# Optimization experiments

Measured on AMD Instinct MI355X. Metric: run time of the kernel, lower is better.

The kernel has to match this reference:

```python
import jax, jax.numpy as jnp
import numpy as np

# QuantizedLinear (BitNet-style ternary weights).
# The original pack_weights/unpack_weights 2-bit round-trip is an identity on the
# ternary values; the nested-loop ternary_matrix_operation is mathematically
# x @ Q^T (weights stored [out, in], accumulating +x[:,i] / -x[:,i] per +-1 entry).

def setup_inputs() -> dict:
    key = jax.random.key(0)
    k1, k2 = jax.random.split(key)
    TOKENS, IN_F, OUT_F = 8192, 4096, 4096
    x = jax.random.normal(k1, (TOKENS, IN_F), dtype=jnp.float32)
    weight = jax.random.normal(k2, (OUT_F, IN_F), dtype=jnp.float32)
    bias = jnp.zeros((OUT_F,), dtype=jnp.float32)
    return {"x": x, "weight": weight, "bias": bias}

def reference(x, weight, bias):
    # absmean ternary quantization: gamma = mean(|W|) + eps
    gamma = jnp.mean(jnp.abs(weight)) + 1e-5
    q = jnp.clip(jnp.round(weight / gamma), -1.0, 1.0)  # ternary {-1,0,1}, [out,in]
    # pack->unpack 2-bit round-trip is identity; loop accumulation == GEMM
    return jnp.einsum('bi,oi->bo', x, q) + bias
```

## Files before the change

kernel.cpp:

```cpp
#include <hip/hip_runtime.h>
#include <stdint.h>


#define M_DIM 8192
#define N_DIM 4096
#define K_DIM 4096
#define BM 256
#define BN 256
#define BK 64

typedef __attribute__((ext_vector_type(4))) int vi4;

#define BAR() asm volatile("s_barrier" ::: "memory")
#define VMW4() asm volatile("s_waitcnt vmcnt(4)" ::: "memory")
#define VMW0() asm volatile("s_waitcnt vmcnt(0)" ::: "memory")
#define SB0() __builtin_amdgcn_sched_barrier(0)
#define LGKM0()                                             \
  do {                                                      \
    SB0();                                                  \
    asm volatile("s_waitcnt lgkmcnt(0)" ::: "memory");      \
    SB0();                                                  \
  } while (0)

__device__ __forceinline__ void load_lds16(const void* g, void* l) {
  __builtin_amdgcn_global_load_lds(
      (const __attribute__((address_space(1))) void*)g,
      (__attribute__((address_space(3))) void*)l,
      16, 0, 0);
}

__global__ __launch_bounds__(256) void k_abs_partial(const float* __restrict__ w,
                                                     double* __restrict__ partial) {
  const int tid = threadIdx.x;
  const size_t base = (size_t)blockIdx.x * 8192 + (size_t)tid * 4;
  double s = 0.0;
#pragma unroll
  for (int it = 0; it < 8; ++it) {
    const float4 v = *reinterpret_cast<const float4*>(w + base + (size_t)it * 1024);
    s += (double)fabsf(v.x) + (double)fabsf(v.y) + (double)fabsf(v.z) + (double)fabsf(v.w);
  }
  __shared__ double sd[256];
  sd[tid] = s;
  __syncthreads();
  for (int off = 128; off > 0; off >>= 1) {
    if (tid < off) sd[tid] += sd[tid + off];
    __syncthreads();
  }
  if (tid == 0) partial[blockIdx.x] = sd[0];
}

__global__ __launch_bounds__(256) void k_abs_final(const double* __restrict__ partial,
                                                   float* __restrict__ gamma_out) {
  const int tid = threadIdx.x;
  double s = 0.0;
  for (int i = tid; i < 2048; i += 256) s += partial[i];
  __shared__ double sd[256];
  sd[tid] = s;
  __syncthreads();
  for (int off = 128; off > 0; off >>= 1) {
    if (tid < off) sd[tid] += sd[tid + off];
    __syncthreads();
  }
  if (tid == 0) {
    float g = (float)(sd[0] / 16777216.0);
    gamma_out[0] = g + 1e-5f;
  }
}

__global__ __launch_bounds__(256) void k_quant(const float* __restrict__ w,
                                               const float* __restrict__ gamma_p,
                                               int* __restrict__ qb) {
  const float g = gamma_p[0];
  const size_t n4 = (size_t)N_DIM * K_DIM / 4;
  const size_t stride = (size_t)gridDim.x * blockDim.x;
  for (size_t i = (size_t)blockIdx.x * blockDim.x + threadIdx.x; i < n4; i += stride) {
    const float4 v = reinterpret_cast<const float4*>(w)[i];
    float r;
    int a, b, c, d;
    r = rintf(v.x / g); a = (r >= 1.0f) ? 1 : ((r <= -1.0f) ? -1 : 0);
    r = rintf(v.y / g); b = (r >= 1.0f) ? 1 : ((r <= -1.0f) ? -1 : 0);
    r = rintf(v.z / g); c = (r >= 1.0f) ? 1 : ((r <= -1.0f) ? -1 : 0);
    r = rintf(v.w / g); d = (r >= 1.0f) ? 1 : ((r <= -1.0f) ? -1 : 0);
    qb[i] = (a & 0xff) | ((b & 0xff) << 8) | ((c & 0xff) << 16) | ((d & 0xff) << 24);
  }
}

__global__ __launch_bounds__(256) void k_quant_x(const float* __restrict__ x,
                                                 signed char* __restrict__ xq,
                                                 float* __restrict__ xs) {
  const int row = blockIdx.x;
  const int tid = threadIdx.x;
  const float* xr = x + (size_t)row * K_DIM;
  float4 v[4];
  float am = 0.0f;
#pragma unroll
  for (int i = 0; i < 4; ++i) {
    v[i] = reinterpret_cast<const float4*>(xr)[tid * 4 + i];
    am = fmaxf(am, fmaxf(fmaxf(fabsf(v[i].x), fabsf(v[i].y)),
                         fmaxf(fabsf(v[i].z), fabsf(v[i].w))));
  }
  for (int off = 32; off > 0; off >>= 1) am = fmaxf(am, __shfl_down(am, off));
  __shared__ float sm[4];
  if ((tid & 63) == 0) sm[tid >> 6] = am;
  __syncthreads();
  const float bm = fmaxf(fmaxf(fmaxf(sm[0], sm[1]), fmaxf(sm[2], sm[3])), 1e-20f);
  if (tid == 0) xs[row] = bm / 127.0f;
  const float inv = 127.0f / bm;
  union { signed char c[16]; int4 q; } u;
#pragma unroll
  for (int i = 0; i < 4; ++i) {
    u.c[i * 4 + 0] = (signed char)(int)rintf(v[i].x * inv);
    u.c[i * 4 + 1] = (signed char)(int)rintf(v[i].y * inv);
    u.c[i * 4 + 2] = (signed char)(int)rintf(v[i].z * inv);
    u.c[i * 4 + 3] = (signed char)(int)rintf(v[i].w * inv);
  }
  *reinterpret_cast<int4*>(xq + (size_t)row * K_DIM + tid * 16) = u.q;
}

__global__ __launch_bounds__(512, 2) void k_gemm(const signed char* __restrict__ Aq,
                                                 const signed char* __restrict__ Bq,
                                                 const float* __restrict__ xs,
                                                 const float* __restrict__ bias,
                                                 float* __restrict__ C) {
  __shared__ unsigned char lds[3][2][256][64];

  const int tid = threadIdx.x;
  const int wid = tid >> 6;
  const int lane = tid & 63;
  const int wm = wid >> 2;
  const int wn = wid & 3;
  const int l15 = lane & 15;
  const int l4 = lane >> 4;

  const int c8 = blockIdx.x & 7;
  const int idx = blockIdx.x >> 3;
  const int bcol = (c8 * 2 + (idx & 1)) * BN;
  const int brow = (idx >> 1) * BM;

  const int srow = wid * 16 + (lane >> 2);
  const int scol = ((lane & 3) ^ ((lane >> 3) & 3)) << 4;
  const int rdoff = ((l4 ^ ((l15 >> 1) & 3)) << 4);

#define STAGE1(buf, op, half, kt)                                                  \
  do {                                                                             \
    const signed char* g =                                                         \
        ((op) ? Bq + (size_t)(bcol + (half)*128 + srow) * K_DIM                    \
              : Aq + (size_t)(brow + (half)*128 + srow) * K_DIM) + (kt)*64 + scol; \
    load_lds16(g, (char*)&lds[buf][op][(half)*128][0] + (size_t)wid * 1024);       \
  } while (0)

#define RD_A(AR, buf, i0)                                                         \
  _Pragma("unroll") for (int i = 0; i < 4; ++i)                                   \
    AR[i] = *reinterpret_cast<const vi4*>(                                        \
        &lds[buf][0][0][0] + (size_t)(wm * 128 + ((i0) + i) * 16 + l15) * 64 + rdoff);
#define RD_B(BR, buf, p0)                                                         \
  _Pragma("unroll") for (int p = 0; p < 2; ++p)                                   \
    BR[p] = *reinterpret_cast<const vi4*>(                                        \
        &lds[buf][1][0][0] + (size_t)(((p0) + p) * 64 + wn * 16 + l15) * 64 + rdoff);

#define MFMAQ(AV, BV, IO, PO)                                                     \
  _Pragma("unroll") for (int i = 0; i < 4; ++i)                                   \
    _Pragma("unroll") for (int p = 0; p < 2; ++p)                                 \
      acc[(IO) + i][(PO) + p] = __builtin_amdgcn_mfma_i32_16x16x64_i8(            \
          AV[i], BV[p], acc[(IO) + i][(PO) + p], 0, 0, 0);

  vi4 acc[8][4];
#pragma unroll
  for (int i = 0; i < 8; ++i)
#pragma unroll
    for (int p = 0; p < 4; ++p)
#pragma unroll
      for (int e = 0; e < 4; ++e) acc[i][p][e] = 0;

  vi4 aL[4], aH[4], bL[2], bH[2];

  STAGE1(0, 0, 0, 0); STAGE1(0, 0, 1, 0); STAGE1(0, 1, 0, 0); STAGE1(0, 1, 1, 0);
  STAGE1(1, 0, 0, 1); STAGE1(1, 0, 1, 1); STAGE1(1, 1, 0, 1); STAGE1(1, 1, 1, 1);
  VMW4();
  BAR();

  int cur = 0;
  for (int t = 0; t < 63; ++t) {
    const int stg = (cur == 0) ? 2 : cur - 1;
    RD_A(aL, cur, 0);
    RD_B(bL, cur, 0);
    SB0();
    if (t < 62) { STAGE1(stg, 0, 0, t + 2); STAGE1(stg, 0, 1, t + 2); }
    BAR();
    LGKM0();
    __builtin_amdgcn_s_setprio(1);
    MFMAQ(aL, bL, 0, 0);
    __builtin_amdgcn_s_setprio(0);
    BAR();
    RD_A(aH, cur, 4);
    RD_B(bH, cur, 2);
    SB0();
    if (t < 62) { STAGE1(stg, 1, 0, t + 2); STAGE1(stg, 1, 1, t + 2); }
    BAR();
    LGKM0();
    __builtin_amdgcn_s_setprio(1);
    MFMAQ(aH, bH, 4, 2);
    MFMAQ(aL, bH, 0, 2);
    MFMAQ(aH, bL, 4, 0);
    __builtin_amdgcn_s_setprio(0);
    if (t < 62) VMW4(); else VMW0();
    BAR();
    cur = (cur == 2) ? 0 : cur + 1;
  }

  RD_A(aL, cur, 0); RD_B(bL, cur, 0);
  RD_A(aH, cur, 4); RD_B(bH, cur, 2);
  LGKM0();
  __builtin_amdgcn_s_setprio(1);
  MFMAQ(aL, bL, 0, 0);
  MFMAQ(aH, bH, 4, 2);
  MFMAQ(aL, bH, 0, 2);
  MFMAQ(aH, bL, 4, 0);
  __builtin_amdgcn_s_setprio(0);

  float bi[4];
#pragma unroll
  for (int p = 0; p < 4; ++p) bi[p] = bias[bcol + p * 64 + wn * 16 + l15];
#pragma unroll
  for (int i = 0; i < 8; ++i) {
#pragma unroll
    for (int j = 0; j < 4; ++j) {
      const int row = brow + wm * 128 + i * 16 + l4 * 4 + j;
      const float sc = xs[row];
      float* crow = C + (size_t)row * N_DIM + bcol + wn * 16 + l15;
#pragma unroll
      for (int p = 0; p < 4; ++p) crow[p * 64] = (float)acc[i][p][j] * sc + bi[p];
    }
  }
#undef STAGE1
#undef RD_A
#undef RD_B
#undef MFMAQ
}

extern "C" void kernel_launch(void* const* d_in, const int* in_sizes, int n_in,
                              void* d_out, int out_size, void* d_ws, size_t ws_size,
                              hipStream_t stream) {
  (void)in_sizes; (void)n_in; (void)out_size; (void)ws_size;
  const float* x = (const float*)d_in[0];
  const float* w = (const float*)d_in[1];
  const float* bias = (const float*)d_in[2];
  float* out = (float*)d_out;

  char* ws = (char*)d_ws;
  signed char* xq = (signed char*)ws;
  signed char* qb = (signed char*)(ws + (size_t)M_DIM * K_DIM);
  float* xs = (float*)(ws + (size_t)M_DIM * K_DIM + (size_t)N_DIM * K_DIM);
  double* partial = (double*)((char*)xs + M_DIM * sizeof(float));
  float* gamma = (float*)(partial + 2048);

  k_abs_partial<<<2048, 256, 0, stream>>>(w, partial);
  k_abs_final<<<1, 256, 0, stream>>>(partial, gamma);
  k_quant<<<2048, 256, 0, stream>>>(w, gamma, (int*)qb);
  k_quant_x<<<M_DIM, 256, 0, stream>>>(x, xq, xs);

  k_gemm<<<512, 512, 0, stream>>>(xq, qb, xs, bias, out);
}
```

Baseline: 202.9 us.

## Load B fragments directly from global into registers, stage only A in LDS

The GEMM no longer stages the ternary weight tile B through LDS. Each wave now loads its own B fragments straight from global memory into registers, double-buffered across k-steps, and only A goes through a triple-buffered LDS ring. The main loop is unrolled by two and each step issues 32 MFMAs per wave, with vmcnt waits retuned to match. This halves LDS traffic and footprint per block, but the per-wave global B loads are strided and uncoalesced, B is re-read by each wm row of waves, and more registers are needed.

```diff
diff --git a/kernel.cpp b/kernel.cpp
--- a/kernel.cpp
+++ b/kernel.cpp
@@ -12,8 +12,7 @@
 typedef __attribute__((ext_vector_type(4))) int vi4;
 
 #define BAR() asm volatile("s_barrier" ::: "memory")
-#define VMW4() asm volatile("s_waitcnt vmcnt(4)" ::: "memory")
-#define VMW0() asm volatile("s_waitcnt vmcnt(0)" ::: "memory")
+#define VMW(n) asm volatile("s_waitcnt vmcnt(" #n ")" ::: "memory")
 #define SB0() __builtin_amdgcn_sched_barrier(0)
 #define LGKM0()                                             \
   do {                                                      \
@@ -122,7 +121,7 @@
                                                  const float* __restrict__ xs,
                                                  const float* __restrict__ bias,
                                                  float* __restrict__ C) {
-  __shared__ unsigned char lds[3][2][256][64];
+  __shared__ unsigned char lds[3][256][64];
 
   const int tid = threadIdx.x;
   const int wid = tid >> 6;
@@ -141,28 +140,43 @@
   const int scol = ((lane & 3) ^ ((lane >> 3) & 3)) << 4;
   const int rdoff = ((l4 ^ ((l15 >> 1) & 3)) << 4);
 
-#define STAGE1(buf, op, half, kt)                                                  \
-  do {                                                                             \
-    const signed char* g =                                                         \
-        ((op) ? Bq + (size_t)(bcol + (half)*128 + srow) * K_DIM                    \
-              : Aq + (size_t)(brow + (half)*128 + srow) * K_DIM) + (kt)*64 + scol; \
-    load_lds16(g, (char*)&lds[buf][op][(half)*128][0] + (size_t)wid * 1024);       \
-  } while (0)
-
-#define RD_A(AR, buf, i0)                                                         \
-  _Pragma("unroll") for (int i = 0; i < 4; ++i)                                   \
-    AR[i] = *reinterpret_cast<const vi4*>(                                        \
-        &lds[buf][0][0][0] + (size_t)(wm * 128 + ((i0) + i) * 16 + l15) * 64 + rdoff);
-#define RD_B(BR, buf, p0)                                                         \
-  _Pragma("unroll") for (int p = 0; p < 2; ++p)                                   \
-    BR[p] = *reinterpret_cast<const vi4*>(                                        \
-        &lds[buf][1][0][0] + (size_t)(((p0) + p) * 64 + wn * 16 + l15) * 64 + rdoff);
-
-#define MFMAQ(AV, BV, IO, PO)                                                     \
-  _Pragma("unroll") for (int i = 0; i < 4; ++i)                                   \
-    _Pragma("unroll") for (int p = 0; p < 2; ++p)                                 \
-      acc[(IO) + i][(PO) + p] = __builtin_amdgcn_mfma_i32_16x16x64_i8(            \
-          AV[i], BV[p], acc[(IO) + i][(PO) + p], 0, 0, 0);
+  const signed char* bbase =
+      Bq + (size_t)(bcol + wn * 16 + l15) * K_DIM + l4 * 16;
+
+#define STAGE_A(buf, kt)                                                           \
+  do {                                                                             \
+    load_lds16(Aq + (size_t)(brow + srow) * K_DIM + (kt)*64 + scol,                \
+               (char*)&lds[buf][0][0] + (size_t)wid * 1024);                       \
+    load_lds16(Aq + (size_t)(brow + 128 + srow) * K_DIM + (kt)*64 + scol,          \
+               (char*)&lds[buf][128][0] + (size_t)wid * 1024);                     \
+    SB0();                                                                         \
+  } while (0)
+
+#define GLB_B(BR, kt)                                                              \
+  do {                                                                             \
+    _Pragma("unroll") for (int p = 0; p < 4; ++p)                                  \
+      BR[p] = *reinterpret_cast<const vi4*>(                                       \
+          bbase + (size_t)(p * 64) * K_DIM + (kt)*64);                             \
+    SB0();                                                                         \
+  } while (0)
+
+#define RD_A8(F, buf)                                                              \
+  do {                                                                             \
+    _Pragma("unroll") for (int i = 0; i < 8; ++i)                                  \
+      F[i] = *reinterpret_cast<const vi4*>(                                        \
+          &lds[buf][0][0] + (size_t)(wm * 128 + i * 16 + l15) * 64 + rdoff);       \
+    SB0();                                                                         \
+  } while (0)
+
+#define MFMA32(F, BR)                                                              \
+  do {                                                                             \
+    __builtin_amdgcn_s_setprio(1);                                                 \
+    _Pragma("unroll") for (int i = 0; i < 8; ++i)                                  \
+      _Pragma("unroll") for (int p = 0; p < 4; ++p)                                \
+        acc[i][p] = __builtin_amdgcn_mfma_i32_16x16x64_i8(F[i], BR[p],             \
+                                                          acc[i][p], 0, 0, 0);     \
+    __builtin_amdgcn_s_setprio(0);                                                 \
+  } while (0)
 
   vi4 acc[8][4];
 #pragma unroll
@@ -172,51 +186,51 @@
 #pragma unroll
       for (int e = 0; e < 4; ++e) acc[i][p][e] = 0;
 
-  vi4 aL[4], aH[4], bL[2], bH[2];
-
-  STAGE1(0, 0, 0, 0); STAGE1(0, 0, 1, 0); STAGE1(0, 1, 0, 0); STAGE1(0, 1, 1, 0);
-  STAGE1(1, 0, 0, 1); STAGE1(1, 0, 1, 1); STAGE1(1, 1, 0, 1); STAGE1(1, 1, 1, 1);
-  VMW4();
+  vi4 fr[8], bA[4], bB[4];
+
+  STAGE_A(0, 0);
+  STAGE_A(1, 1);
+  GLB_B(bA, 0);
+  VMW(0);
   BAR();
 
   int cur = 0;
-  for (int t = 0; t < 63; ++t) {
-    const int stg = (cur == 0) ? 2 : cur - 1;
-    RD_A(aL, cur, 0);
-    RD_B(bL, cur, 0);
-    SB0();
-    if (t < 62) { STAGE1(stg, 0, 0, t + 2); STAGE1(stg, 0, 1, t + 2); }
+  for (int t = 0; t < 62; t += 2) {
+    const int b1 = (cur == 2) ? 0 : cur + 1;
+    const int b2 = (b1 == 2) ? 0 : b1 + 1;
+    RD_A8(fr, cur);
+    GLB_B(bB, t + 1);
+    STAGE_A(b2, t + 2);
+    VMW(8);
+    LGKM0();
+    MFMA32(fr, bA);
+    VMW(6);
     BAR();
+    RD_A8(fr, b1);
+    GLB_B(bA, t + 2);
+    STAGE_A(cur, t + 3);
+    VMW(8);
     LGKM0();
-    __builtin_amdgcn_s_setprio(1);
-    MFMAQ(aL, bL, 0, 0);
-    __builtin_amdgcn_s_setprio(0);
+    MFMA32(fr, bB);
+    VMW(6);
     BAR();
-    RD_A(aH, cur, 4);
-    RD_B(bH, cur, 2);
-    SB0();
-    if (t < 62) { STAGE1(stg, 1, 0, t + 2); STAGE1(stg, 1, 1, t + 2); }
-    BAR();
+    cur = b2;
+  }
+
+  RD_A8(fr, cur);
+  GLB_B(bB, 63);
+  VMW(6);
+  LGKM0();
+  MFMA32(fr, bA);
+  VMW(4);
+  BAR();
+  {
+    const int b1 = (cur == 2) ? 0 : cur + 1;
+    RD_A8(fr, b1);
+    VMW(0);
     LGKM0();
-    __builtin_amdgcn_s_setprio(1);
-    MFMAQ(aH, bH, 4, 2);
-    MFMAQ(aL, bH, 0, 2);
-    MFMAQ(aH, bL, 4, 0);
-    __builtin_amdgcn_s_setprio(0);
-    if (t < 62) VMW4(); else VMW0();
-    BAR();
-    cur = (cur == 2) ? 0 : cur + 1;
-  }
-
-  RD_A(aL, cur, 0); RD_B(bL, cur, 0);
-  RD_A(aH, cur, 4); RD_B(bH, cur, 2);
-  LGKM0();
-  __builtin_amdgcn_s_setprio(1);
-  MFMAQ(aL, bL, 0, 0);
-  MFMAQ(aH, bH, 4, 2);
-  MFMAQ(aL, bH, 0, 2);
-  MFMAQ(aH, bL, 4, 0);
-  __builtin_amdgcn_s_setprio(0);
+    MFMA32(fr, bB);
+  }
 
   float bi[4];
 #pragma unroll
@@ -232,10 +246,10 @@
       for (int p = 0; p < 4; ++p) crow[p * 64] = (float)acc[i][p][j] * sc + bi[p];
     }
   }
-#undef STAGE1
-#undef RD_A
-#undef RD_B
-#undef MFMAQ
+#undef STAGE_A
+#undef GLB_B
+#undef RD_A8
+#undef MFMA32
 }
 
 extern "C" void kernel_launch(void* const* d_in, const int* in_sizes, int n_in,
```

New measurement: 268.6 us. 32.4% more time.

## Shrink GEMM tile to 128x256 with single-phase pipelined K loop

Applied to the files above, without the earlier changes.

Halves the block tile in M from 256 to 128, doubling the grid to 1024 blocks, and rewrites the main loop so each iteration issues all three global-to-LDS loads for the next-but-one stage, reads every fragment once and runs 16 MFMAs. This replaces the earlier two-half split with its extra barriers. Each wave now owns a 64x64 output tile instead of 128x64, which cuts accumulator registers and LDS per block. The cost is lower arithmetic intensity: B tiles are reloaded by twice as many blocks, and the launch_bounds min-blocks hint is dropped.

```diff
diff --git a/kernel.cpp b/kernel.cpp
--- a/kernel.cpp
+++ b/kernel.cpp
@@ -5,15 +5,14 @@
 #define M_DIM 8192
 #define N_DIM 4096
 #define K_DIM 4096
-#define BM 256
+#define BM 128
 #define BN 256
 #define BK 64
 
 typedef __attribute__((ext_vector_type(4))) int vi4;
 
 #define BAR() asm volatile("s_barrier" ::: "memory")
-#define VMW4() asm volatile("s_waitcnt vmcnt(4)" ::: "memory")
-#define VMW0() asm volatile("s_waitcnt vmcnt(0)" ::: "memory")
+#define VMW(n) asm volatile("s_waitcnt vmcnt(" #n ")" ::: "memory")
 #define SB0() __builtin_amdgcn_sched_barrier(0)
 #define LGKM0()                                             \
   do {                                                      \
@@ -117,12 +116,12 @@
   *reinterpret_cast<int4*>(xq + (size_t)row * K_DIM + tid * 16) = u.q;
 }
 
-__global__ __launch_bounds__(512, 2) void k_gemm(const signed char* __restrict__ Aq,
-                                                 const signed char* __restrict__ Bq,
-                                                 const float* __restrict__ xs,
-                                                 const float* __restrict__ bias,
-                                                 float* __restrict__ C) {
-  __shared__ unsigned char lds[3][2][256][64];
+__global__ __launch_bounds__(512) void k_gemm(const signed char* __restrict__ Aq,
+                                              const signed char* __restrict__ Bq,
+                                              const float* __restrict__ xs,
+                                              const float* __restrict__ bias,
+                                              float* __restrict__ C) {
+  __shared__ unsigned char lds[3][24576];
 
   const int tid = threadIdx.x;
   const int wid = tid >> 6;
@@ -137,105 +136,94 @@
   const int bcol = (c8 * 2 + (idx & 1)) * BN;
   const int brow = (idx >> 1) * BM;
 
-  const int srow = wid * 16 + (lane >> 2);
-  const int scol = ((lane & 3) ^ ((lane >> 3) & 3)) << 4;
+  const int srow = tid >> 2;
+  const int scol = ((tid & 3) ^ ((tid >> 3) & 3)) << 4;
   const int rdoff = ((l4 ^ ((l15 >> 1) & 3)) << 4);
 
-#define STAGE1(buf, op, half, kt)                                                  \
-  do {                                                                             \
-    const signed char* g =                                                         \
-        ((op) ? Bq + (size_t)(bcol + (half)*128 + srow) * K_DIM                    \
-              : Aq + (size_t)(brow + (half)*128 + srow) * K_DIM) + (kt)*64 + scol; \
-    load_lds16(g, (char*)&lds[buf][op][(half)*128][0] + (size_t)wid * 1024);       \
-  } while (0)
-
-#define RD_A(AR, buf, i0)                                                         \
-  _Pragma("unroll") for (int i = 0; i < 4; ++i)                                   \
-    AR[i] = *reinterpret_cast<const vi4*>(                                        \
-        &lds[buf][0][0][0] + (size_t)(wm * 128 + ((i0) + i) * 16 + l15) * 64 + rdoff);
-#define RD_B(BR, buf, p0)                                                         \
-  _Pragma("unroll") for (int p = 0; p < 2; ++p)                                   \
-    BR[p] = *reinterpret_cast<const vi4*>(                                        \
-        &lds[buf][1][0][0] + (size_t)(((p0) + p) * 64 + wn * 16 + l15) * 64 + rdoff);
-
-#define MFMAQ(AV, BV, IO, PO)                                                     \
-  _Pragma("unroll") for (int i = 0; i < 4; ++i)                                   \
-    _Pragma("unroll") for (int p = 0; p < 2; ++p)                                 \
-      acc[(IO) + i][(PO) + p] = __builtin_amdgcn_mfma_i32_16x16x64_i8(            \
-          AV[i], BV[p], acc[(IO) + i][(PO) + p], 0, 0, 0);
-
-  vi4 acc[8][4];
-#pragma unroll
-  for (int i = 0; i < 8; ++i)
+#define STAGE_ALL(buf, kt)                                                          \
+  do {                                                                              \
+    load_lds16(Aq + (size_t)(brow + srow) * K_DIM + (kt)*64 + scol,                 \
+               (char*)&lds[buf][0] + (size_t)wid * 1024);                           \
+    load_lds16(Bq + (size_t)(bcol + srow) * K_DIM + (kt)*64 + scol,                 \
+               (char*)&lds[buf][8192] + (size_t)wid * 1024);                        \
+    load_lds16(Bq + (size_t)(bcol + 128 + srow) * K_DIM + (kt)*64 + scol,           \
+               (char*)&lds[buf][16384] + (size_t)wid * 1024);                       \
+    SB0();                                                                          \
+  } while (0)
+
+#define RD8(buf)                                                                    \
+  do {                                                                              \
+    _Pragma("unroll") for (int i = 0; i < 4; ++i)                                   \
+      fa[i] = *reinterpret_cast<const vi4*>(                                        \
+          &lds[buf][0] + (size_t)(wm * 64 + i * 16 + l15) * 64 + rdoff);            \
+    _Pragma("unroll") for (int p = 0; p < 4; ++p)                                   \
+      fb[p] = *reinterpret_cast<const vi4*>(                                        \
+          &lds[buf][8192] + (size_t)(wn * 64 + p * 16 + l15) * 64 + rdoff);         \
+    SB0();                                                                          \
+  } while (0)
+
+#define MFMA16()                                                                    \
+  do {                                                                              \
+    __builtin_amdgcn_s_setprio(1);                                                  \
+    _Pragma("unroll") for (int i = 0; i < 4; ++i)                                   \
+      _Pragma("unroll") for (int p = 0; p < 4; ++p)                                 \
+        acc[i][p] = __builtin_amdgcn_mfma_i32_16x16x64_i8(fa[i], fb[p],             \
+                                                          acc[i][p], 0, 0, 0);      \
+    __builtin_amdgcn_s_setprio(0);                                                  \
+  } while (0)
+
+  vi4 acc[4][4];
+#pragma unroll
+  for (int i = 0; i < 4; ++i)
 #pragma unroll
     for (int p = 0; p < 4; ++p)
 #pragma unroll
       for (int e = 0; e < 4; ++e) acc[i][p][e] = 0;
 
-  vi4 aL[4], aH[4], bL[2], bH[2];
-
-  STAGE1(0, 0, 0, 0); STAGE1(0, 0, 1, 0); STAGE1(0, 1, 0, 0); STAGE1(0, 1, 1, 0);
-  STAGE1(1, 0, 0, 1); STAGE1(1, 0, 1, 1); STAGE1(1, 1, 0, 1); STAGE1(1, 1, 1, 1);
-  VMW4();
+  vi4 fa[4], fb[4];
+
+  STAGE_ALL(0, 0);
+  STAGE_ALL(1, 1);
+  VMW(3);
   BAR();
 
   int cur = 0;
-  for (int t = 0; t < 63; ++t) {
+  for (int t = 0; t < 62; ++t) {
     const int stg = (cur == 0) ? 2 : cur - 1;
-    RD_A(aL, cur, 0);
-    RD_B(bL, cur, 0);
-    SB0();
-    if (t < 62) { STAGE1(stg, 0, 0, t + 2); STAGE1(stg, 0, 1, t + 2); }
-    BAR();
+    RD8(cur);
+    STAGE_ALL(stg, t + 2);
     LGKM0();
-    __builtin_amdgcn_s_setprio(1);
-    MFMAQ(aL, bL, 0, 0);
-    __builtin_amdgcn_s_setprio(0);
-    BAR();
-    RD_A(aH, cur, 4);
-    RD_B(bH, cur, 2);
-    SB0();
-    if (t < 62) { STAGE1(stg, 1, 0, t + 2); STAGE1(stg, 1, 1, t + 2); }
-    BAR();
-    LGKM0();
-    __builtin_amdgcn_s_setprio(1);
-    MFMAQ(aH, bH, 4, 2);
-    MFMAQ(aL, bH, 0, 2);
-    MFMAQ(aH, bL, 4, 0);
-    __builtin_amdgcn_s_setprio(0);
-    if (t < 62) VMW4(); else VMW0();
+    MFMA16();
+    VMW(3);
     BAR();
     cur = (cur == 2) ? 0 : cur + 1;
   }
-
-  RD_A(aL, cur, 0); RD_B(bL, cur, 0);
-  RD_A(aH, cur, 4); RD_B(bH, cur, 2);
+  RD8(cur);
   LGKM0();
-  __builtin_amdgcn_s_setprio(1);
-  MFMAQ(aL, bL, 0, 0);
-  MFMAQ(aH, bH, 4, 2);
-  MFMAQ(aL, bH, 0, 2);
-  MFMAQ(aH, bL, 4, 0);
-  __builtin_amdgcn_s_setprio(0);
+  MFMA16();
+  VMW(0);
+  BAR();
+  RD8(0);
+  LGKM0();
+  MFMA16();
 
   float bi[4];
 #pragma unroll
-  for (int p = 0; p < 4; ++p) bi[p] = bias[bcol + p * 64 + wn * 16 + l15];
-#pragma unroll
-  for (int i = 0; i < 8; ++i) {
+  for (int p = 0; p < 4; ++p) bi[p] = bias[bcol + wn * 64 + p * 16 + l15];
+#pragma unroll
+  for (int i = 0; i < 4; ++i) {
 #pragma unroll
     for (int j = 0; j < 4; ++j) {
-      const int row = brow + wm * 128 + i * 16 + l4 * 4 + j;
+      const int row = brow + wm * 64 + i * 16 + l4 * 4 + j;
       const float sc = xs[row];
-      float* crow = C + (size_t)row * N_DIM + bcol + wn * 16 + l15;
-#pragma unroll
-      for (int p = 0; p < 4; ++p) crow[p * 64] = (float)acc[i][p][j] * sc + bi[p];
+      float* crow = C + (size_t)row * N_DIM + bcol + wn * 64 + l15;
+#pragma unroll
+      for (int p = 0; p < 4; ++p) crow[p * 16] = (float)acc[i][p][j] * sc + bi[p];
     }
   }
-#undef STAGE1
-#undef RD_A
-#undef RD_B
-#undef MFMAQ
+#undef STAGE_ALL
+#undef RD8
+#undef MFMA16
 }
 
 extern "C" void kernel_launch(void* const* d_in, const int* in_sizes, int n_in,
@@ -259,5 +247,5 @@
   k_quant<<<2048, 256, 0, stream>>>(w, gamma, (int*)qb);
   k_quant_x<<<M_DIM, 256, 0, stream>>>(x, xq, xs);
 
-  k_gemm<<<512, 512, 0, stream>>>(xq, qb, xs, bias, out);
-}
+  k_gemm<<<1024, 512, 0, stream>>>(xq, qb, xs, bias, out);
+}
```

Result: slower. 215.1 us (+6.0%).
